# Kernel optimization log

Measured on AMD Instinct MI355X. Metric: run time of the kernel, lower is better.

Reference implementation:

```python
import jax, jax.numpy as jnp
import numpy as np

_PHI = (1.0 + 5.0 ** 0.5) / 2.0
_VS = np.array([[0, 1, _PHI], [0, 1, -_PHI], [0, -1, _PHI], [0, -1, -_PHI],
                [1, _PHI, 0], [1, -_PHI, 0], [-1, _PHI, 0], [-1, -_PHI, 0],
                [_PHI, 0, 1], [_PHI, 0, -1], [-_PHI, 0, 1], [-_PHI, 0, -1]], dtype=np.float32)
_VS = _VS / np.linalg.norm(_VS, axis=-1, keepdims=True)  # 12 icosahedron vertices
_COLOR_COM = np.array([(0, 1, 2, 3, 4, 5), (0, 5, 4, 3, 2, 1), (2, 5, 4, 1, 0, 3), (5, 0, 1, 3, 2, 4),
                       (3, 5, 2, 0, 4, 1), (4, 0, 5, 2, 1, 3), (1, 3, 4, 2, 0, 5), (1, 0, 2, 4, 3, 5),
                       (4, 1, 2, 5, 0, 3), (3, 1, 4, 0, 2, 5), (5, 1, 0, 4, 2, 3), (2, 4, 5, 3, 0, 1)])
_INV = np.argsort(_COLOR_COM, axis=-1)  # inverse perms: scatter_(-1, color_com, W) == gather with _INV
_C2V = np.array([(0, 1), (6, 7), (2, 11), (4, 9), (5, 8), (3, 10)])
_ROLL = np.array([(0, 1, 2, 3, 4, 5), (0, 2, 3, 4, 5, 1), (0, 3, 4, 5, 1, 2), (0, 4, 5, 1, 2, 3), (0, 5, 1, 2, 3, 4)])
_HEADS = 8


def _build_sym(Wp):
    """(..., 18) raw params -> (..., 13, 12, 6) symmetry-expanded weights."""
    lead = Wp.shape[:-1]
    top = jnp.concatenate([Wp[..., 0:1], jnp.repeat(Wp[..., 1:2], 5, axis=-1)], axis=-1)[..., None, :]
    bot = jnp.concatenate([Wp[..., 2:3], jnp.repeat(Wp[..., 3:4], 5, axis=-1)], axis=-1)[..., None, :]
    cen = jnp.concatenate([Wp[..., 4:5], jnp.repeat(Wp[..., 5:6], 5, axis=-1)], axis=-1)[..., None, :]
    sym = Wp[..., 6:18].reshape(lead + (2, 6))[..., _ROLL].reshape(lead + (10, 6))
    W13 = jnp.concatenate([top, bot, sym, cen], axis=-2)  # (..., 13, 6)
    return W13[..., _INV]  # (..., 13, 12, 6): rotated copies via inverse color permutations


def setup_inputs() -> dict:
    key = jax.random.key(0)
    ks = jax.random.split(key, 6)
    bs, V, n, di, do = 1, 2048, 16, 32, 64
    s = 0.05
    return {
        "neighbor_index": jax.random.randint(ks[0], (bs, V, n), 0, V),
        "vertices": jax.random.normal(ks[1], (bs, V, 3), dtype=jnp.float32),
        "feature_map": jax.random.normal(ks[2], (bs, di, V, 6), dtype=jnp.float32),
        "W_dim": jax.random.normal(ks[3], (di + 1, di), dtype=jnp.float32) * s,
        "W": jax.random.normal(ks[4], (do, di, 18), dtype=jnp.float32) * s,
        "W_dir": jax.random.normal(ks[5], (di * _HEADS, 18), dtype=jnp.float32) * s,
    }


def reference(neighbor_index, vertices, feature_map, W_dim, W, W_dir):
    bs, V, n = neighbor_index.shape
    do, di, _ = W.shape
    H = _HEADS
    dph = di // H
    vs = jnp.asarray(_VS)
    c2v = jnp.asarray(_C2V)
    # neighbor direction (normalized)
    neigh = jax.vmap(lambda v, idx: v[idx])(vertices, neighbor_index)  # (bs,V,n,3)
    nd = neigh - vertices[:, :, None, :]
    ndn = nd / jnp.maximum(jnp.linalg.norm(nd, axis=-1, keepdims=True), 1e-12)
    # symmetry-expanded weights
    W_ro = _build_sym(W)       # (do, di, 13, 12, 6)
    Wd_ro = _build_sym(W_dir)  # (di*H, 13, 12, 6)
    # gather neighbor features: (bs, di, V, n, 6)
    nf = jax.vmap(lambda fm, idx: fm[:, idx])(feature_map, neighbor_index)
    # direction features discretized onto the 6 color axes
    de = jnp.einsum('vi,bqni->bqnv', vs, ndn)          # (bs,V,n,12)
    de = de[..., c2v].max(axis=-1)                      # (bs,V,n,6)
    cross = jnp.concatenate([nf, de[:, None]], axis=1)  # (bs, di+1, V, n, 6)
    cross = jnp.einsum('co,bcpni->bopni', W_dim, cross)  # (bs, di, V, n, 6)
    # per-head attention over neighbors
    Wdr = Wd_ro.reshape(H, di, 13, 12, 6).transpose(0, 1, 2, 4, 3)  # (h, c, k, i, r)
    act = jnp.einsum('hckir,bcpni->hbkpnr', Wdr[:, :, :12], cross) / (dph ** 0.5)
    act = jax.nn.softmax(act, axis=-2)                  # softmax over neighbors n
    cross_h = cross.reshape(bs, H, dph, V, n, 6)
    nfm = jnp.einsum('hbkpnr,bhcpni->bhckpir', act, cross_h).reshape(bs, di, 12, V, 6, 12)
    feat = jnp.einsum('dckri,bckpir->bdkpr', W_ro[:, :, :12], nfm)   # (bs,do,12,V,12)
    center = jnp.einsum('dcri,bcpi->bdpr', W_ro[:, :, 12], feature_map)  # (bs,do,V,12)
    ka = feat.sum(axis=2) + center                       # (bs,do,V,12)
    ka = ka[..., c2v].max(axis=-1)                       # (bs,do,V,6)
    return (ka, feature_map)
```

## Files before the change

### kernel.cpp

```cpp
#include <hip/hip_runtime.h>
#include <cstdint>
#include <cstddef>

#define NN 16
#define DI 32
#define DO 64

typedef short bf16x8 __attribute__((ext_vector_type(8)));
typedef short bf16x4 __attribute__((ext_vector_type(4)));
typedef float f32x4 __attribute__((ext_vector_type(4)));

#if defined(__has_builtin)
#  if __has_builtin(__builtin_amdgcn_mfma_f32_16x16x16_bf16)
#    define MFMA_K16(a, b, c) __builtin_amdgcn_mfma_f32_16x16x16_bf16(a, b, c, 0, 0, 0)
#    define HAVE_K16 1
#  elif __has_builtin(__builtin_amdgcn_mfma_f32_16x16x16bf16_1k)
#    define MFMA_K16(a, b, c) __builtin_amdgcn_mfma_f32_16x16x16bf16_1k(a, b, c, 0, 0, 0)
#    define HAVE_K16 1
#  endif
#endif

__device__ __constant__ int c_INV[12][6] = {
  {0,1,2,3,4,5},{0,5,4,3,2,1},{4,3,0,5,2,1},{1,2,4,3,5,0},
  {3,5,2,0,4,1},{1,4,3,5,0,2},{4,0,3,1,2,5},{1,0,2,4,3,5},
  {4,1,2,5,0,3},{3,1,4,0,2,5},{2,1,4,5,3,0},{4,5,0,3,1,2}};
__device__ __constant__ int c_ROLL[5][6] = {
  {0,1,2,3,4,5},{0,2,3,4,5,1},{0,3,4,5,1,2},{0,4,5,1,2,3},{0,5,1,2,3,4}};
__device__ __constant__ float c_VS[12][3] = {
  {0.f, 0.5257311121f, 0.8506508084f},
  {0.f, 0.5257311121f, -0.8506508084f},
  {0.f, -0.5257311121f, 0.8506508084f},
  {0.f, -0.5257311121f, -0.8506508084f},
  {0.5257311121f, 0.8506508084f, 0.f},
  {0.5257311121f, -0.8506508084f, 0.f},
  {-0.5257311121f, 0.8506508084f, 0.f},
  {-0.5257311121f, -0.8506508084f, 0.f},
  {0.8506508084f, 0.f, 0.5257311121f},
  {0.8506508084f, 0.f, -0.5257311121f},
  {-0.8506508084f, 0.f, 0.5257311121f},
  {-0.8506508084f, 0.f, -0.5257311121f}};
__device__ __constant__ int c_C2V[6][2] = {{0,1},{6,7},{2,11},{4,9},{5,8},{3,10}};

__device__ inline unsigned short f2bf(float f) {
  unsigned int u = __float_as_uint(f);
  unsigned int r = (u + 0x7fffu + ((u >> 16) & 1u)) >> 16;
  return (unsigned short)r;
}
__device__ inline float bf2f(unsigned short h) {
  return __uint_as_float(((unsigned int)h) << 16);
}
__device__ inline unsigned int pack2(float a, float b) {
  return (unsigned int)f2bf(a) | ((unsigned int)f2bf(b) << 16);
}

__device__ inline float sym13(const float* __restrict__ w, int k, int j) {
  if (k == 0)  return w[j == 0 ? 0 : 1];
  if (k == 1)  return w[j == 0 ? 2 : 3];
  if (k == 12) return w[j == 0 ? 4 : 5];
  int a = (k - 2) / 5, rr = (k - 2) % 5;
  return w[6 + a * 6 + c_ROLL[rr][j]];
}

__global__ __launch_bounds__(256) void k0_expand(
    const float* __restrict__ W, const float* __restrict__ Wdir,
    const float* __restrict__ fm,
    unsigned short* __restrict__ A_bf,
    unsigned short* __restrict__ W2k,
    unsigned short* __restrict__ Wck,
    unsigned short* __restrict__ fmTbf,
    float* __restrict__ out_fm, int V) {
  int idx = blockIdx.x * 256 + threadIdx.x;
  if (idx < 221184) {
    int row = idx / 192, ci = idx % 192;
    int h = row / 144, k = (row / 12) % 12, r = row % 12;
    int c = ci / 6, i = ci % 6;
    int rt = row >> 4, rl = row & 15;
    int ks = ci >> 5, q = (ci >> 3) & 3, j = ci & 7;
    A_bf[(((rt * 6 + ks) * 4 + q) * 16 + rl) * 8 + j] =
        f2bf(0.5f * sym13(&Wdir[(h * 32 + c) * 18], k, c_INV[r][i]));
  } else if (idx < 1990656) {
    int e = idx - 221184;
    int kr = e / 12288, rem = e % 12288;
    int k = kr / 12, r = kr % 12, d = rem / 192, ci = rem % 192;
    int c = ci / 6, i = ci % 6;
    int ks = ci >> 5, q = (ci >> 3) & 3, j = ci & 7;
    W2k[kr * 12288 + ((ks * 4 + q) * 64 + d) * 8 + j] =
        f2bf(sym13(&W[(d * 32 + c) * 18], k, c_INV[r][i]));
  } else if (idx < 2138112) {
    int e = idx - 1990656;
    int r = e / 12288, rem = e % 12288, d = rem / 192, ci = rem % 192;
    int c = ci / 6, i = ci % 6;
    int ks = ci >> 5, q = (ci >> 3) & 3, j = ci & 7;
    Wck[r * 12288 + ((ks * 4 + q) * 64 + d) * 8 + j] =
        f2bf(sym13(&W[(d * 32 + c) * 18], 12, c_INV[r][i]));
  } else {
    int e = idx - 2138112;
    if (e < 192 * V) {
      int p = e / 192, ci = e % 192, c = ci / 6, i = ci % 6;
      float v = fm[(c * V + p) * 6 + i];
      fmTbf[e] = f2bf(v);
      out_fm[(c * V + p) * 6 + i] = v;
    }
  }
}

__global__ __launch_bounds__(256) void k1_cross(
    const int* __restrict__ nbi, const float* __restrict__ verts,
    const float* __restrict__ fm, const float* __restrict__ Wdim,
    unsigned short* __restrict__ cross_n,
    unsigned short* __restrict__ crossT_g, int V) {
  __shared__ float in_s[NN * 33 * 6];
  __shared__ float wd_s[33 * 32];
  __shared__ unsigned int cross_u[1536];
  __shared__ int nb_s[NN];
  int p = blockIdx.x, t = threadIdx.x;
  if (t < NN) nb_s[t] = nbi[p * NN + t];
  for (int idx = t; idx < 1056; idx += 256) wd_s[idx] = Wdim[idx];
  __syncthreads();
  for (int idx = t; idx < NN * 32; idx += 256) {
    int n = idx >> 5, c = idx & 31;
    const float* src = fm + ((size_t)c * V + nb_s[n]) * 6;
    float2 a  = *(const float2*)(src + 0);
    float2 b  = *(const float2*)(src + 2);
    float2 cd = *(const float2*)(src + 4);
    float* d = &in_s[(n * 33 + c) * 6];
    d[0] = a.x; d[1] = a.y; d[2] = b.x; d[3] = b.y; d[4] = cd.x; d[5] = cd.y;
  }
  if (t < NN) {
    int n = t, nb = nb_s[n];
    float px = verts[p * 3 + 0], py = verts[p * 3 + 1], pz = verts[p * 3 + 2];
    float dx = verts[nb * 3 + 0] - px, dy = verts[nb * 3 + 1] - py, dz = verts[nb * 3 + 2] - pz;
    float L = sqrtf(dx * dx + dy * dy + dz * dz);
    float inv = 1.0f / fmaxf(L, 1e-12f);
    dx *= inv; dy *= inv; dz *= inv;
    float de[12];
    #pragma unroll
    for (int v = 0; v < 12; ++v)
      de[v] = c_VS[v][0] * dx + c_VS[v][1] * dy + c_VS[v][2] * dz;
    #pragma unroll
    for (int j = 0; j < 6; ++j)
      in_s[(n * 33 + 32) * 6 + j] = fmaxf(de[c_C2V[j][0]], de[c_C2V[j][1]]);
  }
  __syncthreads();
  for (int idx = t; idx < 1536; idx += 256) {
    int n = idx / 96, cp2 = idx % 96;
    int ci0 = cp2 * 2, ci1 = ci0 + 1;
    int o0 = ci0 / 6, i0 = ci0 % 6;
    int o1 = ci1 / 6, i1 = ci1 % 6;
    float s0 = 0.f, s1 = 0.f;
    #pragma unroll
    for (int c = 0; c <= 32; ++c) {
      float f0 = in_s[(n * 33 + c) * 6 + i0];
      float f1 = in_s[(n * 33 + c) * 6 + i1];
      s0 = fmaf(wd_s[c * 32 + o0], f0, s0);
      s1 = fmaf(wd_s[c * 32 + o1], f1, s1);
    }
    cross_u[idx] = (unsigned int)f2bf(s0) | ((unsigned int)f2bf(s1) << 16);
  }
  __syncthreads();
  {
    const uint4* src = (const uint4*)cross_u;
    uint4* d1 = (uint4*)(cross_n + (size_t)p * 3072);
    for (int idx = t; idx < 384; idx += 256) d1[idx] = src[idx];
  }
  {
    unsigned int* d2 = (unsigned int*)(crossT_g + (size_t)p * 3072);
    for (int idx = t; idx < 1536; idx += 256) {
      int np = idx / 192, ci = idx % 192;
      unsigned int u0 = cross_u[(2 * np) * 96 + (ci >> 1)];
      unsigned int u1 = cross_u[(2 * np + 1) * 96 + (ci >> 1)];
      unsigned int h0 = (ci & 1) ? (u0 >> 16) : (u0 & 0xffffu);
      unsigned int h1 = (ci & 1) ? (u1 & 0xffff0000u) : (u1 << 16);
      d2[ci * 8 + np] = h0 | h1;
    }
  }
}

__global__ __launch_bounds__(512, 4) void k2_main(
    const unsigned short* __restrict__ A_bf,
    const unsigned short* __restrict__ cross_n,
    const unsigned short* __restrict__ crossT_g,
    unsigned short* __restrict__ nfm, int V) {
#ifdef HAVE_K16
  __shared__ __align__(16) unsigned short crossT[4][192][16];
#else
  __shared__ __align__(16) unsigned short crossT[4][192][40];
#endif
  int t = threadIdx.x;
  int w = t >> 6, lane = t & 63;
  int quad = lane >> 4, col = lane & 15;
  int p0 = blockIdx.x * 4;
  int pw = w & 1, tw = w >> 1;

  bf16x8 Afr[2][6];
  #pragma unroll
  for (int pi = 0; pi < 2; ++pi)
    #pragma unroll
    for (int ks = 0; ks < 6; ++ks)
      Afr[pi][ks] = *(const bf16x8*)(cross_n + (size_t)(p0 + pw * 2 + pi) * 3072 +
                                     col * 192 + ks * 32 + quad * 8);

#ifdef HAVE_K16
  for (int idx = t; idx < 1536; idx += 512) {
    *(uint4*)&((unsigned short*)crossT)[idx * 8] =
        *(const uint4*)(crossT_g + (size_t)p0 * 3072 + idx * 8);
  }
#else
  for (int idx = t; idx < 1536; idx += 512) {
    int p = idx / 384, rem = idx % 384, ci = rem >> 1, half = rem & 1;
    *(uint4*)&crossT[p][ci][half * 8] =
        *(const uint4*)(crossT_g + (size_t)(p0 + p) * 3072 + ci * 16 + half * 8);
  }
  for (int idx = t; idx < 1536; idx += 512) {
    int p = idx / 384, rem = idx % 384, ci = rem >> 1, half = rem & 1;
    *(uint4*)&crossT[p][ci][16 + half * 8] = make_uint4(0u, 0u, 0u, 0u);
  }
#endif
  __syncthreads();

#ifndef HAVE_K16
  int s0l = quad * 32 + col;
  int s1l = s0l + 16;
#endif

  for (int rt = tw; rt < 72; rt += 4) {
    int h = rt / 9;
    f32x4 acc[2];
    acc[0] = (f32x4){0.f, 0.f, 0.f, 0.f};
    acc[1] = (f32x4){0.f, 0.f, 0.f, 0.f};
    const unsigned short* Abase = A_bf + rt * 3072 + quad * 128 + col * 8;
    #pragma unroll
    for (int ks = 0; ks < 6; ++ks) {
      bf16x8 wf = *(const bf16x8*)(Abase + ks * 512);
      acc[0] = __builtin_amdgcn_mfma_f32_16x16x32_bf16(Afr[0][ks], wf, acc[0], 0, 0, 0);
      acc[1] = __builtin_amdgcn_mfma_f32_16x16x32_bf16(Afr[1][ks], wf, acc[1], 0, 0, 0);
    }
    int row0 = h * 24 + col;
    int row1 = min(h * 24 + 16 + col, 191);
    #pragma unroll
    for (int pi = 0; pi < 2; ++pi) {
      int p_i = pw * 2 + pi;
      float v0 = acc[pi][0], v1 = acc[pi][1], v2 = acc[pi][2], v3 = acc[pi][3];
      float mx = fmaxf(fmaxf(v0, v1), fmaxf(v2, v3));
      mx = fmaxf(mx, __shfl_xor(mx, 16));
      mx = fmaxf(mx, __shfl_xor(mx, 32));
      float e0 = __expf(v0 - mx), e1 = __expf(v1 - mx);
      float e2 = __expf(v2 - mx), e3 = __expf(v3 - mx);
      float s = (e0 + e1) + (e2 + e3);
      s += __shfl_xor(s, 16);
      s += __shfl_xor(s, 32);
      float inv = __builtin_amdgcn_rcpf(s);
      unsigned int lo = pack2(e0 * inv, e1 * inv);
      unsigned int hi = pack2(e2 * inv, e3 * inv);
      f32x4 o0 = (f32x4){0.f, 0.f, 0.f, 0.f}, o1 = o0;
#ifdef HAVE_K16
      union { uint2 u; bf16x4 v; } bcvt;
      bcvt.u = make_uint2(lo, hi);
      bf16x4 a0 = *(const bf16x4*)&crossT[p_i][row0][quad * 4];
      bf16x4 a1 = *(const bf16x4*)&crossT[p_i][row1][quad * 4];
      o0 = MFMA_K16(a0, bcvt.v, o0);
      o1 = MFMA_K16(a1, bcvt.v, o1);
#else
      unsigned int b0 = (unsigned int)__shfl((int)lo, s0l);
      unsigned int b1 = (unsigned int)__shfl((int)hi, s0l);
      unsigned int b2 = (unsigned int)__shfl((int)lo, s1l);
      unsigned int b3 = (unsigned int)__shfl((int)hi, s1l);
      bool vq = (quad < 2);
      union { uint4 u; bf16x8 v; } cvt;
      cvt.u = make_uint4(vq ? b0 : 0u, vq ? b1 : 0u, vq ? b2 : 0u, vq ? b3 : 0u);
      bf16x8 a0 = *(const bf16x8*)&crossT[p_i][row0][quad * 8];
      bf16x8 a1 = *(const bf16x8*)&crossT[p_i][row1][quad * 8];
      o0 = __builtin_amdgcn_mfma_f32_16x16x32_bf16(a0, cvt.v, o0, 0, 0, 0);
      o1 = __builtin_amdgcn_mfma_f32_16x16x32_bf16(a1, cvt.v, o1, 0, 0, 0);
#endif
      size_t rowbase = (size_t)blockIdx.x * 110592 + (size_t)(rt * 16 + col) * 96 + p_i * 24;
      uint2 w0;
      w0.x = pack2(o0[0], o0[1]);
      w0.y = pack2(o0[2], o0[3]);
      *(uint2*)(nfm + rowbase + quad * 4) = w0;
      if (quad < 2) {
        uint2 w1;
        w1.x = pack2(o1[0], o1[1]);
        w1.y = pack2(o1[2], o1[3]);
        *(uint2*)(nfm + rowbase + 16 + quad * 4) = w1;
      }
    }
  }
}

__global__ __launch_bounds__(512) void k3_feat(
    const unsigned short* __restrict__ W2k,
    const unsigned short* __restrict__ Wck,
    const unsigned short* __restrict__ fmTbf,
    const unsigned short* __restrict__ nfm,
    float* __restrict__ out, int V) {
  __shared__ float red[2][3][32][64];
  int pb = blockIdx.x, j = blockIdx.y;
  int t = threadIdx.x, w = t >> 6, lane = t & 63;
  int rhalf = w >> 2, kw = w & 3;
  int r = c_C2V[j][rhalf];
  int quad = lane >> 4, col = lane & 15;
  int p0 = pb * 32;
  f32x4 acc[4][2];
  #pragma unroll
  for (int m = 0; m < 4; ++m)
    #pragma unroll
    for (int jj = 0; jj < 2; ++jj) acc[m][jj] = (f32x4){0.f, 0.f, 0.f, 0.f};

  int base24[6];
  #pragma unroll
  for (int ks = 0; ks < 6; ++ks) {
    int ci = ks * 32 + quad * 8;
    int hh = ci / 24, oo = ci - hh * 24;
    base24[ks] = hh * 13824 + oo;
  }

  int pA = p0 + col, pB = p0 + 16 + col;
  const unsigned short* Bn0 = nfm + (size_t)(pA >> 2) * 110592 + (pA & 3) * 24;
  const unsigned short* Bn1 = nfm + (size_t)(pB >> 2) * 110592 + (pB & 3) * 24;
  const unsigned short* Bc0 = fmTbf + (size_t)pA * 192;
  const unsigned short* Bc1 = fmTbf + (size_t)pB * 192;

  int nkb = (kw == 3) ? 4 : 3;
  for (int i = 0; i < nkb; ++i) {
    int kb = kw * 3 + i;
    const unsigned short* Ab;
    int kr96 = 0;
    if (kb < 12) { Ab = W2k + (size_t)(kb * 12 + r) * 12288; kr96 = (kb * 12 + r) * 96; }
    else         { Ab = Wck + (size_t)r * 12288; }
    const unsigned short* Albase = Ab + quad * 512 + col * 8;
    #pragma unroll
    for (int ks = 0; ks < 6; ++ks) {
      bf16x8 b0, b1;
      if (kb < 12) {
        b0 = *(const bf16x8*)(Bn0 + base24[ks] + kr96);
        b1 = *(const bf16x8*)(Bn1 + base24[ks] + kr96);
      } else {
        int ko = ks * 32 + quad * 8;
        b0 = *(const bf16x8*)(Bc0 + ko);
        b1 = *(const bf16x8*)(Bc1 + ko);
      }
      #pragma unroll
      for (int m = 0; m < 4; ++m) {
        bf16x8 a = *(const bf16x8*)(Albase + ks * 2048 + m * 128);
        acc[m][0] = __builtin_amdgcn_mfma_f32_16x16x32_bf16(a, b0, acc[m][0], 0, 0, 0);
        acc[m][1] = __builtin_amdgcn_mfma_f32_16x16x32_bf16(a, b1, acc[m][1], 0, 0, 0);
      }
    }
  }
  if (kw > 0) {
    #pragma unroll
    for (int m = 0; m < 4; ++m)
      #pragma unroll
      for (int jj = 0; jj < 2; ++jj)
        #pragma unroll
        for (int rr = 0; rr < 4; ++rr)
          red[rhalf][kw - 1][m * 8 + jj * 4 + rr][lane] = acc[m][jj][rr];
  }
  __syncthreads();
  if (kw == 0) {
    #pragma unroll
    for (int m = 0; m < 4; ++m)
      #pragma unroll
      for (int jj = 0; jj < 2; ++jj)
        #pragma unroll
        for (int rr = 0; rr < 4; ++rr) {
          int ri = m * 8 + jj * 4 + rr;
          acc[m][jj][rr] += red[rhalf][0][ri][lane] + red[rhalf][1][ri][lane] + red[rhalf][2][ri][lane];
        }
  }
  if (w == 4) {
    #pragma unroll
    for (int m = 0; m < 4; ++m)
      #pragma unroll
      for (int jj = 0; jj < 2; ++jj)
        #pragma unroll
        for (int rr = 0; rr < 4; ++rr)
          red[1][0][m * 8 + jj * 4 + rr][lane] = acc[m][jj][rr];
  }
  __syncthreads();
  if (w == 0) {
    #pragma unroll
    for (int m = 0; m < 4; ++m)
      #pragma unroll
      for (int jj = 0; jj < 2; ++jj)
        #pragma unroll
        for (int rr = 0; rr < 4; ++rr) {
          float v = fmaxf(acc[m][jj][rr], red[1][0][m * 8 + jj * 4 + rr][lane]);
          int d = m * 16 + quad * 4 + rr;
          int p = p0 + jj * 16 + col;
          out[((size_t)d * V + p) * 6 + j] = v;
        }
  }
}

extern "C" void kernel_launch(void* const* d_in, const int* in_sizes, int n_in,
                              void* d_out, int out_size, void* d_ws, size_t ws_size,
                              hipStream_t stream) {
  const int* nbi = (const int*)d_in[0];
  const float* verts = (const float*)d_in[1];
  const float* fm = (const float*)d_in[2];
  const float* Wdim = (const float*)d_in[3];
  const float* W = (const float*)d_in[4];
  const float* Wdir = (const float*)d_in[5];
  float* out = (float*)d_out;
  float* ws = (float*)d_ws;
  int V = in_sizes[0] / NN;

  unsigned short* A_bf  = (unsigned short*)ws;
  unsigned short* W2k   = (unsigned short*)(ws + 110592);
  unsigned short* Wck   = (unsigned short*)(ws + 995328);
  unsigned short* fmTbf = (unsigned short*)(ws + 1069056);
  size_t o = 1069056 + (size_t)96 * V;
  unsigned short* cross_n = (unsigned short*)(ws + o);
  o += (size_t)1536 * V;
  unsigned short* crossT_g = (unsigned short*)(ws + o);
  o += (size_t)1536 * V;
  unsigned short* nfm = (unsigned short*)(ws + o);

  int n0 = 2138112 + 192 * V;
  k0_expand<<<(n0 + 255) / 256, 256, 0, stream>>>(W, Wdir, fm, A_bf, W2k, Wck, fmTbf,
                                                  out + (size_t)DO * V * 6, V);
  k1_cross<<<V, 256, 0, stream>>>(nbi, verts, fm, Wdim, cross_n, crossT_g, V);
  k2_main<<<V / 4, 512, 0, stream>>>(A_bf, cross_n, crossT_g, nfm, V);
  k3_feat<<<dim3(V / 32, 6), 512, 0, stream>>>(W2k, Wck, fmTbf, nfm, out, V);
}
```

Measured before the change: 180.2 us.

## Compute cross projection with bf16 MFMA, one wave per vertex, packed bf16 converts

The W_dim projection in k1_cross moves from scalar FMA over fp32 shared-memory tiles to bf16 MFMA. Each wave now handles one vertex, with W_dim pre-swizzled into an MFMA B-fragment layout in k0, and the two output layouts are produced from a transposed LDS buffer. Software bf16 rounding is replaced by the hardware packed convert instruction where it is available. The gathered features and the direction term are now quantised to bf16 before the projection, which adds rounding error. The change also depends on barrier-free per-wave LDS use guarded only by waitcnt.

```diff
diff --git a/kernel.cpp b/kernel.cpp
--- a/kernel.cpp
+++ b/kernel.cpp
@@ -17,6 +17,9 @@
 #  elif __has_builtin(__builtin_amdgcn_mfma_f32_16x16x16bf16_1k)
 #    define MFMA_K16(a, b, c) __builtin_amdgcn_mfma_f32_16x16x16bf16_1k(a, b, c, 0, 0, 0)
 #    define HAVE_K16 1
+#  endif
+#  if __has_builtin(__builtin_amdgcn_cvt_pk_bf16_f32)
+#    define HAVE_PKBF 1
 #  endif
 #endif
 
@@ -46,11 +49,18 @@
   unsigned int r = (u + 0x7fffu + ((u >> 16) & 1u)) >> 16;
   return (unsigned short)r;
 }
-__device__ inline float bf2f(unsigned short h) {
-  return __uint_as_float(((unsigned int)h) << 16);
-}
-__device__ inline unsigned int pack2(float a, float b) {
+__device__ inline unsigned int pk2(float a, float b) {
+#ifdef HAVE_PKBF
+  typedef __bf16 bf16v2 __attribute__((ext_vector_type(2)));
+  union { bf16v2 v; unsigned int u; } cv;
+  cv.v = __builtin_amdgcn_cvt_pk_bf16_f32(a, b);
+  return cv.u;
+#else
   return (unsigned int)f2bf(a) | ((unsigned int)f2bf(b) << 16);
+#endif
+}
+__device__ inline unsigned short f2bf_fast(float a) {
+  return (unsigned short)(pk2(a, a) & 0xffffu);
 }
 
 __device__ inline float sym13(const float* __restrict__ w, int k, int j) {
@@ -63,11 +73,12 @@
 
 __global__ __launch_bounds__(256) void k0_expand(
     const float* __restrict__ W, const float* __restrict__ Wdir,
-    const float* __restrict__ fm,
+    const float* __restrict__ fm, const float* __restrict__ Wdim,
     unsigned short* __restrict__ A_bf,
     unsigned short* __restrict__ W2k,
     unsigned short* __restrict__ Wck,
     unsigned short* __restrict__ fmTbf,
+    unsigned short* __restrict__ wdB,
     float* __restrict__ out_fm, int V) {
   int idx = blockIdx.x * 256 + threadIdx.x;
   if (idx < 221184) {
@@ -77,7 +88,7 @@
     int rt = row >> 4, rl = row & 15;
     int ks = ci >> 5, q = (ci >> 3) & 3, j = ci & 7;
     A_bf[(((rt * 6 + ks) * 4 + q) * 16 + rl) * 8 + j] =
-        f2bf(0.5f * sym13(&Wdir[(h * 32 + c) * 18], k, c_INV[r][i]));
+        f2bf_fast(0.5f * sym13(&Wdir[(h * 32 + c) * 18], k, c_INV[r][i]));
   } else if (idx < 1990656) {
     int e = idx - 221184;
     int kr = e / 12288, rem = e % 12288;
@@ -85,93 +96,137 @@
     int c = ci / 6, i = ci % 6;
     int ks = ci >> 5, q = (ci >> 3) & 3, j = ci & 7;
     W2k[kr * 12288 + ((ks * 4 + q) * 64 + d) * 8 + j] =
-        f2bf(sym13(&W[(d * 32 + c) * 18], k, c_INV[r][i]));
+        f2bf_fast(sym13(&W[(d * 32 + c) * 18], k, c_INV[r][i]));
   } else if (idx < 2138112) {
     int e = idx - 1990656;
     int r = e / 12288, rem = e % 12288, d = rem / 192, ci = rem % 192;
     int c = ci / 6, i = ci % 6;
     int ks = ci >> 5, q = (ci >> 3) & 3, j = ci & 7;
     Wck[r * 12288 + ((ks * 4 + q) * 64 + d) * 8 + j] =
-        f2bf(sym13(&W[(d * 32 + c) * 18], 12, c_INV[r][i]));
+        f2bf_fast(sym13(&W[(d * 32 + c) * 18], 12, c_INV[r][i]));
+  } else if (idx < 2138112 + 192 * V) {
+    int e = idx - 2138112;
+    int p = e / 192, ci = e % 192, c = ci / 6, i = ci % 6;
+    float v = fm[(c * V + p) * 6 + i];
+    fmTbf[e] = f2bf_fast(v);
+    out_fm[(c * V + p) * 6 + i] = v;
   } else {
-    int e = idx - 2138112;
-    if (e < 192 * V) {
-      int p = e / 192, ci = e % 192, c = ci / 6, i = ci % 6;
-      float v = fm[(c * V + p) * 6 + i];
-      fmTbf[e] = f2bf(v);
-      out_fm[(c * V + p) * 6 + i] = v;
+    int e = idx - (2138112 + 192 * V);
+    if (e < 2048) {
+      int j = e & 7, lane = (e >> 3) & 63, kc = (e >> 9) & 1, ot = e >> 10;
+      int k = kc * 32 + (lane >> 4) * 8 + j;
+      int o = ot * 16 + (lane & 15);
+      wdB[e] = (k <= 32) ? f2bf_fast(Wdim[k * 32 + o]) : (unsigned short)0;
     }
   }
 }
 
 __global__ __launch_bounds__(256) void k1_cross(
     const int* __restrict__ nbi, const float* __restrict__ verts,
-    const float* __restrict__ fm, const float* __restrict__ Wdim,
+    const float* __restrict__ fm, const unsigned short* __restrict__ wdB,
     unsigned short* __restrict__ cross_n,
     unsigned short* __restrict__ crossT_g, int V) {
-  __shared__ float in_s[NN * 33 * 6];
-  __shared__ float wd_s[33 * 32];
-  __shared__ unsigned int cross_u[1536];
-  __shared__ int nb_s[NN];
-  int p = blockIdx.x, t = threadIdx.x;
-  if (t < NN) nb_s[t] = nbi[p * NN + t];
-  for (int idx = t; idx < 1056; idx += 256) wd_s[idx] = Wdim[idx];
-  __syncthreads();
-  for (int idx = t; idx < NN * 32; idx += 256) {
-    int n = idx >> 5, c = idx & 31;
-    const float* src = fm + ((size_t)c * V + nb_s[n]) * 6;
-    float2 a  = *(const float2*)(src + 0);
-    float2 b  = *(const float2*)(src + 2);
-    float2 cd = *(const float2*)(src + 4);
-    float* d = &in_s[(n * 33 + c) * 6];
-    d[0] = a.x; d[1] = a.y; d[2] = b.x; d[3] = b.y; d[4] = cd.x; d[5] = cd.y;
-  }
-  if (t < NN) {
-    int n = t, nb = nb_s[n];
-    float px = verts[p * 3 + 0], py = verts[p * 3 + 1], pz = verts[p * 3 + 2];
-    float dx = verts[nb * 3 + 0] - px, dy = verts[nb * 3 + 1] - py, dz = verts[nb * 3 + 2] - pz;
-    float L = sqrtf(dx * dx + dy * dy + dz * dz);
-    float inv = 1.0f / fmaxf(L, 1e-12f);
-    dx *= inv; dy *= inv; dz *= inv;
-    float de[12];
-    #pragma unroll
-    for (int v = 0; v < 12; ++v)
-      de[v] = c_VS[v][0] * dx + c_VS[v][1] * dy + c_VS[v][2] * dz;
-    #pragma unroll
-    for (int j = 0; j < 6; ++j)
-      in_s[(n * 33 + 32) * 6 + j] = fmaxf(de[c_C2V[j][0]], de[c_C2V[j][1]]);
-  }
-  __syncthreads();
-  for (int idx = t; idx < 1536; idx += 256) {
-    int n = idx / 96, cp2 = idx % 96;
-    int ci0 = cp2 * 2, ci1 = ci0 + 1;
-    int o0 = ci0 / 6, i0 = ci0 % 6;
-    int o1 = ci1 / 6, i1 = ci1 % 6;
-    float s0 = 0.f, s1 = 0.f;
-    #pragma unroll
-    for (int c = 0; c <= 32; ++c) {
-      float f0 = in_s[(n * 33 + c) * 6 + i0];
-      float f1 = in_s[(n * 33 + c) * 6 + i1];
-      s0 = fmaf(wd_s[c * 32 + o0], f0, s0);
-      s1 = fmaf(wd_s[c * 32 + o1], f1, s1);
-    }
-    cross_u[idx] = (unsigned int)f2bf(s0) | ((unsigned int)f2bf(s1) << 16);
-  }
-  __syncthreads();
+  __shared__ __align__(16) unsigned short in_bf[4][96][64];
+  int t = threadIdx.x, w = t >> 6, lane = t & 63;
+  int quad = lane >> 4, col = lane & 15;
+  int p = blockIdx.x * 4 + w;
+  unsigned short* mybuf = &in_bf[w][0][0];
+
+  for (int z = lane; z < 384; z += 64) {
+    int m = z >> 2, q = z & 3;
+    *(uint4*)&mybuf[m * 64 + 32 + q * 8] = make_uint4(0u, 0u, 0u, 0u);
+  }
+
+  float px = verts[p * 3 + 0], py = verts[p * 3 + 1], pz = verts[p * 3 + 2];
+  for (int idx = lane; idx < 528; idx += 64) {
+    int n = idx / 33, c = idx - n * 33;
+    int nb = nbi[p * 16 + n];
+    if (c < 32) {
+      const float* src = fm + ((size_t)c * V + nb) * 6;
+      float2 a  = *(const float2*)(src + 0);
+      float2 b  = *(const float2*)(src + 2);
+      float2 cd = *(const float2*)(src + 4);
+      unsigned short* dst = &mybuf[(n * 6) * 64 + c];
+      dst[0 * 64] = f2bf_fast(a.x);
+      dst[1 * 64] = f2bf_fast(a.y);
+      dst[2 * 64] = f2bf_fast(b.x);
+      dst[3 * 64] = f2bf_fast(b.y);
+      dst[4 * 64] = f2bf_fast(cd.x);
+      dst[5 * 64] = f2bf_fast(cd.y);
+    } else {
+      float qx = verts[nb * 3 + 0] - px;
+      float qy = verts[nb * 3 + 1] - py;
+      float qz = verts[nb * 3 + 2] - pz;
+      float L = sqrtf(qx * qx + qy * qy + qz * qz);
+      float inv = 1.0f / fmaxf(L, 1e-12f);
+      qx *= inv; qy *= inv; qz *= inv;
+      float de[12];
+      #pragma unroll
+      for (int v = 0; v < 12; ++v)
+        de[v] = c_VS[v][0] * qx + c_VS[v][1] * qy + c_VS[v][2] * qz;
+      #pragma unroll
+      for (int j = 0; j < 6; ++j)
+        mybuf[(n * 6 + j) * 64 + 32] = f2bf_fast(fmaxf(de[c_C2V[j][0]], de[c_C2V[j][1]]));
+    }
+  }
+
+  bf16x8 Bf[2][2];
+  #pragma unroll
+  for (int ot = 0; ot < 2; ++ot)
+    #pragma unroll
+    for (int kc = 0; kc < 2; ++kc)
+      Bf[ot][kc] = *(const bf16x8*)(wdB + (size_t)((ot * 2 + kc) * 64 + lane) * 8);
+
+  asm volatile("s_waitcnt lgkmcnt(0)" ::: "memory");
+
+  f32x4 D[6][2];
+  #pragma unroll
+  for (int mt = 0; mt < 6; ++mt) {
+    bf16x8 a0 = *(const bf16x8*)&mybuf[(mt * 16 + col) * 64 + quad * 8];
+    bf16x8 a1 = *(const bf16x8*)&mybuf[(mt * 16 + col) * 64 + 32 + quad * 8];
+    #pragma unroll
+    for (int ot = 0; ot < 2; ++ot) {
+      f32x4 acc = (f32x4){0.f, 0.f, 0.f, 0.f};
+      acc = __builtin_amdgcn_mfma_f32_16x16x32_bf16(a0, Bf[ot][0], acc, 0, 0, 0);
+      acc = __builtin_amdgcn_mfma_f32_16x16x32_bf16(a1, Bf[ot][1], acc, 0, 0, 0);
+      D[mt][ot] = acc;
+    }
+  }
+
+  asm volatile("s_waitcnt lgkmcnt(0)" ::: "memory");
+  unsigned short* crossL = mybuf;
+  #pragma unroll
+  for (int mt = 0; mt < 6; ++mt) {
+    #pragma unroll
+    for (int ot = 0; ot < 2; ++ot) {
+      #pragma unroll
+      for (int r = 0; r < 4; ++r) {
+        int m = mt * 16 + quad * 4 + r;
+        int n = m / 6, i = m - n * 6;
+        int ci = (ot * 16 + col) * 6 + i;
+        crossL[ci * 16 + n] = f2bf_fast(D[mt][ot][r]);
+      }
+    }
+  }
+  asm volatile("s_waitcnt lgkmcnt(0)" ::: "memory");
+
   {
-    const uint4* src = (const uint4*)cross_u;
-    uint4* d1 = (uint4*)(cross_n + (size_t)p * 3072);
-    for (int idx = t; idx < 384; idx += 256) d1[idx] = src[idx];
+    uint4* ct = (uint4*)(crossT_g + (size_t)p * 3072);
+    const uint4* cl4 = (const uint4*)crossL;
+    for (int q = lane; q < 384; q += 64) ct[q] = cl4[q];
   }
   {
-    unsigned int* d2 = (unsigned int*)(crossT_g + (size_t)p * 3072);
-    for (int idx = t; idx < 1536; idx += 256) {
-      int np = idx / 192, ci = idx % 192;
-      unsigned int u0 = cross_u[(2 * np) * 96 + (ci >> 1)];
-      unsigned int u1 = cross_u[(2 * np + 1) * 96 + (ci >> 1)];
-      unsigned int h0 = (ci & 1) ? (u0 >> 16) : (u0 & 0xffffu);
-      unsigned int h1 = (ci & 1) ? (u1 & 0xffff0000u) : (u1 << 16);
-      d2[ci * 8 + np] = h0 | h1;
+    uint4* cn = (uint4*)(cross_n + (size_t)p * 3072);
+    for (int q = lane; q < 384; q += 64) {
+      int n = (q * 8) / 192, ci0 = (q * 8) % 192;
+      unsigned int u[4];
+      #pragma unroll
+      for (int h2 = 0; h2 < 4; ++h2) {
+        unsigned int lo = crossL[(ci0 + 2 * h2 + 0) * 16 + n];
+        unsigned int hi = crossL[(ci0 + 2 * h2 + 1) * 16 + n];
+        u[h2] = lo | (hi << 16);
+      }
+      cn[q] = make_uint4(u[0], u[1], u[2], u[3]);
     }
   }
 }
@@ -250,8 +305,8 @@
       s += __shfl_xor(s, 16);
       s += __shfl_xor(s, 32);
       float inv = __builtin_amdgcn_rcpf(s);
-      unsigned int lo = pack2(e0 * inv, e1 * inv);
-      unsigned int hi = pack2(e2 * inv, e3 * inv);
+      unsigned int lo = pk2(e0 * inv, e1 * inv);
+      unsigned int hi = pk2(e2 * inv, e3 * inv);
       f32x4 o0 = (f32x4){0.f, 0.f, 0.f, 0.f}, o1 = o0;
 #ifdef HAVE_K16
       union { uint2 u; bf16x4 v; } bcvt;
@@ -275,13 +330,13 @@
 #endif
       size_t rowbase = (size_t)blockIdx.x * 110592 + (size_t)(rt * 16 + col) * 96 + p_i * 24;
       uint2 w0;
-      w0.x = pack2(o0[0], o0[1]);
-      w0.y = pack2(o0[2], o0[3]);
+      w0.x = pk2(o0[0], o0[1]);
+      w0.y = pk2(o0[2], o0[3]);
       *(uint2*)(nfm + rowbase + quad * 4) = w0;
       if (quad < 2) {
         uint2 w1;
-        w1.x = pack2(o1[0], o1[1]);
-        w1.y = pack2(o1[2], o1[3]);
+        w1.x = pk2(o1[0], o1[1]);
+        w1.y = pk2(o1[2], o1[3]);
         *(uint2*)(nfm + rowbase + 16 + quad * 4) = w1;
       }
     }
@@ -417,11 +472,13 @@
   unsigned short* crossT_g = (unsigned short*)(ws + o);
   o += (size_t)1536 * V;
   unsigned short* nfm = (unsigned short*)(ws + o);
-
-  int n0 = 2138112 + 192 * V;
-  k0_expand<<<(n0 + 255) / 256, 256, 0, stream>>>(W, Wdir, fm, A_bf, W2k, Wck, fmTbf,
-                                                  out + (size_t)DO * V * 6, V);
-  k1_cross<<<V, 256, 0, stream>>>(nbi, verts, fm, Wdim, cross_n, crossT_g, V);
+  o += (size_t)13824 * V;
+  unsigned short* wdB = (unsigned short*)(ws + o);
+
+  int n0 = 2138112 + 192 * V + 2048;
+  k0_expand<<<(n0 + 255) / 256, 256, 0, stream>>>(W, Wdir, fm, Wdim, A_bf, W2k, Wck, fmTbf,
+                                                  wdB, out + (size_t)DO * V * 6, V);
+  k1_cross<<<V / 4, 256, 0, stream>>>(nbi, verts, fm, wdB, cross_n, crossT_g, V);
   k2_main<<<V / 4, 512, 0, stream>>>(A_bf, cross_n, crossT_g, nfm, V);
   k3_feat<<<dim3(V / 32, 6), 512, 0, stream>>>(W2k, Wck, fmTbf, nfm, out, V);
 }
```

Measured after the change: 178.7 us. About the same (-0.8%).
